# Kernel tuning notes

Hardware: AMD Instinct MI355X
Metric: run time of the kernel (lower is better)

The kernel has to match this reference:

```python
import jax, jax.numpy as jnp
import numpy as np
from jax import lax

BLANK = 27
NEG = -1e30  # safe -inf substitute (avoids NaN grads through logaddexp)


def _joint_log_probs(enc, dec, We, Wd, bf, Wp, bp):
    # Concat-then-Linear == sum of per-branch matmuls: [e;d] @ Wf = e@We + d@Wd.
    f = jnp.einsum('bte,eh->bth', enc, We)          # [B,T,H]
    g = jnp.einsum('bud,dh->buh', dec, Wd)          # [B,U1,H]
    h = jnp.tanh(f[:, :, None, :] + g[:, None, :, :] + bf)  # [B,T,U1,H]
    logits = jnp.einsum('btuh,hv->btuv', h, Wp) + bp         # [B,T,U1,V]
    return jax.nn.log_softmax(logits, axis=-1)


def _rnnt_loss_one(lp, tgt, t_len, u_len):
    # lp: [T,U1,V] log-probs, tgt: [U] int labels, t_len/u_len: scalars.
    T, U1, V = lp.shape
    blank_lp = lp[:, :, BLANK]                                   # [T,U1]
    lab_lp = jnp.take_along_axis(lp[:, :U1 - 1, :],
                                 tgt[None, :, None], axis=2)[..., 0]  # [T,U]

    # alpha[0,:] : only label emissions along u at t=0.
    alpha0 = jnp.concatenate([jnp.zeros((1,), lp.dtype),
                              jnp.cumsum(lab_lp[0])])            # [U1]

    def step(prev_alpha, inp):
        b_prev, lab_t = inp                       # [U1], [U]
        from_below = prev_alpha + b_prev          # blank move from t-1
        first = from_below[0]

        def inner(carry, x):
            fb, lab = x
            new = jnp.logaddexp(fb, carry + lab)  # blank-from-below vs label-from-left
            return new, new

        _, rest = lax.scan(inner, first, (from_below[1:], lab_t))
        alpha_t = jnp.concatenate([first[None], rest])
        return alpha_t, alpha_t

    _, alphas = lax.scan(step, alpha0, (blank_lp[:-1], lab_lp[1:]))
    alpha = jnp.concatenate([alpha0[None], alphas], axis=0)      # [T,U1]

    # Terminal: emit final blank at (t_len-1, u_len).
    return -(alpha[t_len - 1, u_len] + blank_lp[t_len - 1, u_len])


def setup_inputs() -> dict:
    key = jax.random.key(0)
    ks = jax.random.split(key, 10)
    B, T, U, E, D, H, V = 8, 400, 60, 256, 256, 512, 28
    enc_state = jax.random.normal(ks[0], (B, T, E), jnp.float32)
    dec_state = jax.random.normal(ks[1], (B, U + 1, D), jnp.float32)
    targets = jax.random.randint(ks[2], (B, U), 0, BLANK, jnp.int32)
    inputs_length = jax.random.randint(ks[3], (B,), 200, T + 1, jnp.int32)
    targets_length = jax.random.randint(ks[4], (B,), 30, U + 1, jnp.int32)
    s1 = 1.0 / np.sqrt(E + D)
    s2 = 1.0 / np.sqrt(H)
    We = jax.random.normal(ks[5], (E, H), jnp.float32) * s1
    Wd = jax.random.normal(ks[6], (D, H), jnp.float32) * s1
    bf = jax.random.normal(ks[7], (H,), jnp.float32) * s1
    Wp = jax.random.normal(ks[8], (H, V), jnp.float32) * s2
    bp = jax.random.normal(ks[9], (V,), jnp.float32) * s2
    return {"enc_state": enc_state, "dec_state": dec_state,
            "We": We, "Wd": Wd, "bf": bf, "Wp": Wp, "bp": bp,
            "targets": targets, "inputs_length": inputs_length,
            "targets_length": targets_length}


def reference(enc_state, dec_state, We, Wd, bf, Wp, bp,
              targets, inputs_length, targets_length):
    lp = _joint_log_probs(enc_state, dec_state, We, Wd, bf, Wp, bp)
    loss = jax.vmap(_rnnt_loss_one)(lp, targets, inputs_length, targets_length)
    return loss  # [B], reduction='none'
```

## Files before the change

### kernel.cpp

```cpp
#include <hip/hip_runtime.h>
#include <hip/hip_bf16.h>
#include <math.h>

#define NEGF (-1e30f)
#define LOG2E 1.4426950408889634f
#define LN2F 0.6931471805599453f
#define TSCALE 2.885390081777927f

typedef __attribute__((ext_vector_type(8))) short bf16x8;
typedef __attribute__((ext_vector_type(4))) float f32x4;

#define DROWS_PAD 480
#define DPITCH 64
#define PF 16

__device__ __forceinline__ unsigned short f2bf(float x) {
    __hip_bfloat16 h = __float2bfloat16(x);
    return *reinterpret_cast<unsigned short*>(&h);
}

__device__ __forceinline__ float wave_shr1(float x) {
    int i = __builtin_bit_cast(int, x);
    int r = __builtin_amdgcn_update_dpp(0, i, 0x138, 0xf, 0xf, true);
    return __builtin_bit_cast(float, r);
}

__device__ __forceinline__ float4 rcp4_nr(float4 d) {
    float4 y;
    y.x = __builtin_bit_cast(float, 0x7EF311C3 - __builtin_bit_cast(int, d.x));
    y.y = __builtin_bit_cast(float, 0x7EF311C3 - __builtin_bit_cast(int, d.y));
    y.z = __builtin_bit_cast(float, 0x7EF311C3 - __builtin_bit_cast(int, d.z));
    y.w = __builtin_bit_cast(float, 0x7EF311C3 - __builtin_bit_cast(int, d.w));
    float4 t;
    t.x = fmaf(-d.x, y.x, 2.f); t.y = fmaf(-d.y, y.y, 2.f);
    t.z = fmaf(-d.z, y.z, 2.f); t.w = fmaf(-d.w, y.w, 2.f);
    y.x *= t.x; y.y *= t.y; y.z *= t.z; y.w *= t.w;
    return y;
}

__global__ __launch_bounds__(256) void k_pack(const float* __restrict__ We,
                                              const float* __restrict__ Wd,
                                              const float* __restrict__ Wp,
                                              const float* __restrict__ bp,
                                              unsigned short* __restrict__ WeFrag,
                                              unsigned short* __restrict__ WdFrag,
                                              unsigned short* __restrict__ BfragP,
                                              float* __restrict__ csbp) {
    int gid = blockIdx.x * 256 + threadIdx.x;
    if (gid < 32768) {
        const float* W = (gid < 16384) ? We : Wd;
        unsigned short* F = (gid < 16384) ? WeFrag : WdFrag;
        int s = gid & 16383;
        int lane = s & 63;
        int c = (s >> 6) & 7;
        int nt = s >> 9;
        int n = nt * 16 + (lane & 15);
        int kbase = c * 32 + ((lane >> 4) & 3) * 8;
        unsigned short* dst = F + (size_t)s * 8;
#pragma unroll
        for (int j = 0; j < 8; ++j) dst[j] = f2bf(W[(size_t)(kbase + j) * 512 + n]);
    } else if (gid < 34816) {
        int s = gid - 32768;
        int lane = s & 63;
        int half = (s >> 6) & 1;
        int c = s >> 7;
        int n = half * 16 + (lane & 15);
        int kbase = c * 32 + (lane >> 4) * 8;
        unsigned short* dst = BfragP + (size_t)s * 8;
#pragma unroll
        for (int j = 0; j < 8; ++j) {
            float v = (n < 28) ? (-2.f * Wp[(kbase + j) * 28 + n]) : 0.f;
            dst[j] = f2bf(v);
        }
    } else if (gid < 34848) {
        int v = gid - 34816;
        float s = 0.f;
        if (v < 28) {
            for (int k = 0; k < 512; ++k) s += Wp[k * 28 + v];
            s += bp[v];
        }
        csbp[v] = s;
    }
}

__global__ __launch_bounds__(256) void k_gemm(const float* __restrict__ enc,
                                              const float* __restrict__ dec,
                                              const float* __restrict__ bfv,
                                              const unsigned short* __restrict__ WeFrag,
                                              const unsigned short* __restrict__ WdFrag,
                                              float* __restrict__ f,
                                              float* __restrict__ g) {
    const int wid = blockIdx.x * 4 + threadIdx.y;
    const int lane = threadIdx.x;
    const int m16 = lane & 15;
    const int quad = lane >> 4;

    const float* A; const unsigned short* WF; float* Out; int M, rt, ct; bool isg;
    if (wid < 1600) { A = enc; WF = WeFrag; Out = f; M = 3200; rt = wid >> 3; ct = wid & 7; isg = false; }
    else { int w2 = wid - 1600; A = dec; WF = WdFrag; Out = g; M = 488; rt = w2 >> 3; ct = w2 & 7; isg = true; }

    const int row = rt * 16 + m16;
    const float* arow = A + (size_t)min(row, M - 1) * 256 + quad * 8;

    f32x4 acc[4];
#pragma unroll
    for (int i = 0; i < 4; ++i) acc[i] = (f32x4){0.f, 0.f, 0.f, 0.f};

#pragma unroll
    for (int c = 0; c < 8; ++c) {
        float4 a0 = *(const float4*)(arow + c * 32);
        float4 a1 = *(const float4*)(arow + c * 32 + 4);
        union { unsigned short s[8]; bf16x8 v; } Af;
        Af.s[0] = f2bf(a0.x); Af.s[1] = f2bf(a0.y);
        Af.s[2] = f2bf(a0.z); Af.s[3] = f2bf(a0.w);
        Af.s[4] = f2bf(a1.x); Af.s[5] = f2bf(a1.y);
        Af.s[6] = f2bf(a1.z); Af.s[7] = f2bf(a1.w);
#pragma unroll
        for (int i = 0; i < 4; ++i) {
            int nt = ct * 4 + i;
            bf16x8 Bv = *(const bf16x8*)(WF + (size_t)((nt * 8 + c) * 64 + lane) * 8);
            acc[i] = __builtin_amdgcn_mfma_f32_16x16x32_bf16(Af.v, Bv, acc[i], 0, 0, 0);
        }
    }

#pragma unroll
    for (int i = 0; i < 4; ++i) {
        int n = ct * 64 + i * 16 + m16;
        float bv = isg ? bfv[n] : 0.f;
#pragma unroll
        for (int r = 0; r < 4; ++r) {
            int ro = rt * 16 + quad * 4 + r;
            if (ro < M) Out[(size_t)ro * 512 + n] = (acc[i][r] + bv) * TSCALE;
        }
    }
}

__global__ __launch_bounds__(256, 4) void k_cells(const float* __restrict__ f,
                                                  const float* __restrict__ g,
                                                  const unsigned short* __restrict__ Bfrag,
                                                  const float* __restrict__ csbp,
                                                  const int* __restrict__ targets,
                                                  const int* __restrict__ ilen,
                                                  const int* __restrict__ ulenp,
                                                  float2* __restrict__ pairD) {
    const int b = blockIdx.z;
    const int tlen = ilen[b];
    const int t0 = blockIdx.x * 16;
    if (t0 >= tlen) return;
    if ((int)blockIdx.y * 4 > ulenp[b]) return;
    const int wave = threadIdx.y;
    const int lane = threadIdx.x;
    const int u_raw = blockIdx.y * 4 + wave;
    const int u = min(u_raw, 60);
    const int tid = wave * 64 + lane;

    __shared__ float fs[16 * 516];

    {
        const float4* src = (const float4*)(f + (size_t)(b * 400 + t0) * 512);
#pragma unroll
        for (int i = 0; i < 8; ++i) {
            int idx = tid + i * 256;
            int row = idx >> 7;
            int c4 = idx & 127;
            float4 v = src[idx];
            *(float4*)&fs[row * 516 + c4 * 4] = v;
        }
    }
    __syncthreads();

    const int quad = lane >> 4;
    const int m16 = lane & 15;
    const float* gu = g + (size_t)(b * 61 + u) * 512 + quad * 8;
    const float* fsrow = fs + m16 * 516 + quad * 8;
    f32x4 acc0 = {0.f, 0.f, 0.f, 0.f};
    f32x4 acc1 = {0.f, 0.f, 0.f, 0.f};
    const float4 one4 = make_float4(1.f, 1.f, 1.f, 1.f);

    float4 FA[2], FB[2], GA[2], GB[2];
    bf16x8 BR0[2], BR1[2];
    FA[0] = *(const float4*)(fsrow);
    FB[0] = *(const float4*)(fsrow + 4);
    GA[0] = *(const float4*)(gu);
    GB[0] = *(const float4*)(gu + 4);
    BR0[0] = *(const bf16x8*)(Bfrag + ((size_t)(0 * 64 + lane)) * 8);
    BR1[0] = *(const bf16x8*)(Bfrag + ((size_t)(1 * 64 + lane)) * 8);

#pragma unroll
    for (int c = 0; c < 16; ++c) {
        const int cu = c & 1;
        const int nx = cu ^ 1;
        if (c < 15) {
            FA[nx] = *(const float4*)(fsrow + (c + 1) * 32);
            FB[nx] = *(const float4*)(fsrow + (c + 1) * 32 + 4);
            GA[nx] = *(const float4*)(gu + (c + 1) * 32);
            GB[nx] = *(const float4*)(gu + (c + 1) * 32 + 4);
            BR0[nx] = *(const bf16x8*)(Bfrag + ((size_t)(((c + 1) * 2 + 0) * 64 + lane)) * 8);
            BR1[nx] = *(const bf16x8*)(Bfrag + ((size_t)(((c + 1) * 2 + 1) * 64 + lane)) * 8);
        }
        float4 s0 = FA[cu] + GA[cu];
        float4 s1 = FB[cu] + GB[cu];
        float4 e0, e1;
        e0.x = __builtin_amdgcn_exp2f(s0.x); e0.y = __builtin_amdgcn_exp2f(s0.y);
        e0.z = __builtin_amdgcn_exp2f(s0.z); e0.w = __builtin_amdgcn_exp2f(s0.w);
        e1.x = __builtin_amdgcn_exp2f(s1.x); e1.y = __builtin_amdgcn_exp2f(s1.y);
        e1.z = __builtin_amdgcn_exp2f(s1.z); e1.w = __builtin_amdgcn_exp2f(s1.w);
        float4 r0 = rcp4_nr(e0 + one4);
        float4 r1 = rcp4_nr(e1 + one4);
        union { unsigned short s[8]; bf16x8 v; } A;
        A.s[0] = f2bf(r0.x); A.s[1] = f2bf(r0.y);
        A.s[2] = f2bf(r0.z); A.s[3] = f2bf(r0.w);
        A.s[4] = f2bf(r1.x); A.s[5] = f2bf(r1.y);
        A.s[6] = f2bf(r1.z); A.s[7] = f2bf(r1.w);
        acc0 = __builtin_amdgcn_mfma_f32_16x16x32_bf16(A.v, BR0[cu], acc0, 0, 0, 0);
        acc1 = __builtin_amdgcn_mfma_f32_16x16x32_bf16(A.v, BR1[cu], acc1, 0, 0, 0);
    }

    float cs0 = csbp[m16];
    int n1 = 16 + m16;
    bool n1v = (n1 < 28);
    float cs1 = csbp[n1 & 31];
    int tv = targets[b * 60 + min(u, 59)];

    float res_blank[4], res_lab[4];
#pragma unroll
    for (int r = 0; r < 4; ++r) {
        float l0 = acc0[r] + cs0;
        float l1 = n1v ? (acc1[r] + cs1) : NEGF;
        float mx = fmaxf(l0, l1);
        mx = fmaxf(mx, __shfl_xor(mx, 1, 64));
        mx = fmaxf(mx, __shfl_xor(mx, 2, 64));
        mx = fmaxf(mx, __shfl_xor(mx, 4, 64));
        mx = fmaxf(mx, __shfl_xor(mx, 8, 64));
        float s = __builtin_amdgcn_exp2f((l0 - mx) * LOG2E) +
                  __builtin_amdgcn_exp2f((l1 - mx) * LOG2E);
        s += __shfl_xor(s, 1, 64);
        s += __shfl_xor(s, 2, 64);
        s += __shfl_xor(s, 4, 64);
        s += __shfl_xor(s, 8, 64);
        float lse = mx + __logf(s);
        int base = lane & 48;
        float labsrc = (tv < 16) ? l0 : l1;
        float labv = __shfl(labsrc, base | (tv & 15), 64);
        float blankv = __shfl(l1, base | 11, 64);
        res_blank[r] = (blankv - lse) * LOG2E;
        res_lab[r] = (labv - lse) * LOG2E;
    }

    if (m16 == 0 && u_raw <= 60) {
        float2* Pd = pairD + (size_t)b * (DROWS_PAD * DPITCH);
#pragma unroll
        for (int r = 0; r < 4; ++r) {
            int t = t0 + quad * 4 + r;
            if (t < tlen) {
                int d = t + u;
                float2 pr;
                pr.x = res_blank[r];
                pr.y = (u <= 59) ? res_lab[r] : NEGF;
                Pd[d * DPITCH + u] = pr;
            }
        }
    }
}

__global__ __launch_bounds__(64) void k_alpha(const float2* __restrict__ pairD,
                                              const int* __restrict__ ilen,
                                              const int* __restrict__ ulenp,
                                              float* __restrict__ out) {
    const int b = blockIdx.x;
    const int u = threadIdx.x;
    const float2* Pd = pairD + (size_t)b * (DROWS_PAD * DPITCH);
    const int tl = ilen[b];
    const int ul = ulenp[b];
    const int dstar = tl - 1 + ul;
    const int dmax = ((dstar + PF - 1) / PF) * PF;
    const bool uok = (u <= 60);
    const bool lok = (u >= 1 && u <= 60);

    float cur = (u == 0) ? 0.f : NEGF;
    float saved = NEGF, savedBlank = NEGF;

    float2 pf[PF];
#pragma unroll
    for (int i = 0; i < PF; ++i) pf[i] = Pd[i * DPITCH + u];

    for (int d0 = 1; d0 <= dmax; d0 += PF) {
#pragma unroll
        for (int i = 0; i < PF; ++i) {
            const int d = d0 + i;
            float2 v = pf[i];
            pf[i] = Pd[(d + PF - 1) * DPITCH + u];
            int t = d - u;
            float bv = (t >= 1 && t <= 399 && uok) ? v.x : NEGF;
            float lvn = wave_shr1(v.y);
            float lv = (lok && t >= 0 && t <= 399) ? lvn : NEGF;
            float up = wave_shr1(cur);
            float a = cur + bv;
            float c2 = up + lv;
            float mx = fmaxf(a, c2), mn = fminf(a, c2);
            float nv = mx + __log2f(1.f + __builtin_amdgcn_exp2f(mn - mx));
            bool valid = (t >= 0 && t <= 399 && uok);
            cur = valid ? nv : cur;
            saved = (d == dstar) ? cur : saved;
            savedBlank = (d == dstar) ? v.x : savedBlank;
        }
    }
    if (u == ul) out[b] = -(saved + savedBlank) * LN2F;
}

extern "C" void kernel_launch(void* const* d_in, const int* in_sizes, int n_in,
                              void* d_out, int out_size, void* d_ws, size_t ws_size,
                              hipStream_t stream) {
    const float* enc = (const float*)d_in[0];
    const float* dec = (const float*)d_in[1];
    const float* We  = (const float*)d_in[2];
    const float* Wd  = (const float*)d_in[3];
    const float* bf  = (const float*)d_in[4];
    const float* Wp  = (const float*)d_in[5];
    const float* bp  = (const float*)d_in[6];
    const int* targets = (const int*)d_in[7];
    const int* ilen    = (const int*)d_in[8];
    const int* ulen    = (const int*)d_in[9];
    float* out = (float*)d_out;
    float* ws = (float*)d_ws;

    float* f     = ws;
    float* g     = ws + 1638400;
    unsigned short* BfragP = (unsigned short*)(ws + 1888256);
    unsigned short* WeFrag = (unsigned short*)(ws + 1896448);
    unsigned short* WdFrag = (unsigned short*)(ws + 1961984);
    float* csbp  = ws + 2027520;
    float2* pairD = (float2*)(ws + 2027552);

    k_pack<<<137, 256, 0, stream>>>(We, Wd, Wp, bp, WeFrag, WdFrag, BfragP, csbp);

    k_gemm<<<462, dim3(64, 4, 1), 0, stream>>>(enc, dec, bf, WeFrag, WdFrag, f, g);

    dim3 gridC(25, 16, 8);
    dim3 blockC(64, 4, 1);
    k_cells<<<gridC, blockC, 0, stream>>>(f, g, BfragP, csbp, targets, ilen, ulen, pairD);

    k_alpha<<<8, 64, 0, stream>>>(pairD, ilen, ulen, out);
}
```

Before: 148.8 us.

## Reuse staged f tile across 16 u per block; two-step alpha diagonal recurrence

k_cells now has each block loop over four groups of 4 u-values, so the 16x512 f tile staged in shared memory is reused for 16 u instead of 4. The grid's y-dimension shrinks from 16 to 4 to match. This cuts redundant global-to-LDS loads of f but leaves fewer blocks in flight and adds a serial loop inside each block. k_alpha now advances two anti-diagonals per step with a three-term logsumexp, roughly halving the serial dependency chain at the cost of more arithmetic per step, and it special-cases the terminal diagonal.

```diff
diff --git a/kernel.cpp b/kernel.cpp
--- a/kernel.cpp
+++ b/kernel.cpp
@@ -145,13 +145,12 @@
                                                   float2* __restrict__ pairD) {
     const int b = blockIdx.z;
     const int tlen = ilen[b];
+    const int ulen = ulenp[b];
     const int t0 = blockIdx.x * 16;
     if (t0 >= tlen) return;
-    if ((int)blockIdx.y * 4 > ulenp[b]) return;
+    if ((int)blockIdx.y * 16 > ulen) return;
     const int wave = threadIdx.y;
     const int lane = threadIdx.x;
-    const int u_raw = blockIdx.y * 4 + wave;
-    const int u = min(u_raw, 60);
     const int tid = wave * 64 + lane;
 
     __shared__ float fs[16 * 516];
@@ -171,93 +170,101 @@
 
     const int quad = lane >> 4;
     const int m16 = lane & 15;
-    const float* gu = g + (size_t)(b * 61 + u) * 512 + quad * 8;
     const float* fsrow = fs + m16 * 516 + quad * 8;
-    f32x4 acc0 = {0.f, 0.f, 0.f, 0.f};
-    f32x4 acc1 = {0.f, 0.f, 0.f, 0.f};
     const float4 one4 = make_float4(1.f, 1.f, 1.f, 1.f);
-
-    float4 FA[2], FB[2], GA[2], GB[2];
-    bf16x8 BR0[2], BR1[2];
-    FA[0] = *(const float4*)(fsrow);
-    FB[0] = *(const float4*)(fsrow + 4);
-    GA[0] = *(const float4*)(gu);
-    GB[0] = *(const float4*)(gu + 4);
-    BR0[0] = *(const bf16x8*)(Bfrag + ((size_t)(0 * 64 + lane)) * 8);
-    BR1[0] = *(const bf16x8*)(Bfrag + ((size_t)(1 * 64 + lane)) * 8);
-
-#pragma unroll
-    for (int c = 0; c < 16; ++c) {
-        const int cu = c & 1;
-        const int nx = cu ^ 1;
-        if (c < 15) {
-            FA[nx] = *(const float4*)(fsrow + (c + 1) * 32);
-            FB[nx] = *(const float4*)(fsrow + (c + 1) * 32 + 4);
-            GA[nx] = *(const float4*)(gu + (c + 1) * 32);
-            GB[nx] = *(const float4*)(gu + (c + 1) * 32 + 4);
-            BR0[nx] = *(const bf16x8*)(Bfrag + ((size_t)(((c + 1) * 2 + 0) * 64 + lane)) * 8);
-            BR1[nx] = *(const bf16x8*)(Bfrag + ((size_t)(((c + 1) * 2 + 1) * 64 + lane)) * 8);
-        }
-        float4 s0 = FA[cu] + GA[cu];
-        float4 s1 = FB[cu] + GB[cu];
-        float4 e0, e1;
-        e0.x = __builtin_amdgcn_exp2f(s0.x); e0.y = __builtin_amdgcn_exp2f(s0.y);
-        e0.z = __builtin_amdgcn_exp2f(s0.z); e0.w = __builtin_amdgcn_exp2f(s0.w);
-        e1.x = __builtin_amdgcn_exp2f(s1.x); e1.y = __builtin_amdgcn_exp2f(s1.y);
-        e1.z = __builtin_amdgcn_exp2f(s1.z); e1.w = __builtin_amdgcn_exp2f(s1.w);
-        float4 r0 = rcp4_nr(e0 + one4);
-        float4 r1 = rcp4_nr(e1 + one4);
-        union { unsigned short s[8]; bf16x8 v; } A;
-        A.s[0] = f2bf(r0.x); A.s[1] = f2bf(r0.y);
-        A.s[2] = f2bf(r0.z); A.s[3] = f2bf(r0.w);
-        A.s[4] = f2bf(r1.x); A.s[5] = f2bf(r1.y);
-        A.s[6] = f2bf(r1.z); A.s[7] = f2bf(r1.w);
-        acc0 = __builtin_amdgcn_mfma_f32_16x16x32_bf16(A.v, BR0[cu], acc0, 0, 0, 0);
-        acc1 = __builtin_amdgcn_mfma_f32_16x16x32_bf16(A.v, BR1[cu], acc1, 0, 0, 0);
-    }
-
-    float cs0 = csbp[m16];
-    int n1 = 16 + m16;
-    bool n1v = (n1 < 28);
-    float cs1 = csbp[n1 & 31];
-    int tv = targets[b * 60 + min(u, 59)];
-
-    float res_blank[4], res_lab[4];
-#pragma unroll
-    for (int r = 0; r < 4; ++r) {
-        float l0 = acc0[r] + cs0;
-        float l1 = n1v ? (acc1[r] + cs1) : NEGF;
-        float mx = fmaxf(l0, l1);
-        mx = fmaxf(mx, __shfl_xor(mx, 1, 64));
-        mx = fmaxf(mx, __shfl_xor(mx, 2, 64));
-        mx = fmaxf(mx, __shfl_xor(mx, 4, 64));
-        mx = fmaxf(mx, __shfl_xor(mx, 8, 64));
-        float s = __builtin_amdgcn_exp2f((l0 - mx) * LOG2E) +
-                  __builtin_amdgcn_exp2f((l1 - mx) * LOG2E);
-        s += __shfl_xor(s, 1, 64);
-        s += __shfl_xor(s, 2, 64);
-        s += __shfl_xor(s, 4, 64);
-        s += __shfl_xor(s, 8, 64);
-        float lse = mx + __logf(s);
-        int base = lane & 48;
-        float labsrc = (tv < 16) ? l0 : l1;
-        float labv = __shfl(labsrc, base | (tv & 15), 64);
-        float blankv = __shfl(l1, base | 11, 64);
-        res_blank[r] = (blankv - lse) * LOG2E;
-        res_lab[r] = (labv - lse) * LOG2E;
-    }
-
-    if (m16 == 0 && u_raw <= 60) {
-        float2* Pd = pairD + (size_t)b * (DROWS_PAD * DPITCH);
+    const float cs0 = csbp[m16];
+    const int n1 = 16 + m16;
+    const bool n1v = (n1 < 28);
+    const float cs1 = csbp[n1 & 31];
+    float2* Pd = pairD + (size_t)b * (DROWS_PAD * DPITCH);
+
+    for (int ub = 0; ub < 4; ++ub) {
+        const int ubase = blockIdx.y * 16 + ub * 4;
+        if (ubase > ulen) break;
+        const int u_raw = ubase + wave;
+        const int u = min(u_raw, 60);
+        const float* gu = g + (size_t)(b * 61 + u) * 512 + quad * 8;
+
+        f32x4 acc0 = {0.f, 0.f, 0.f, 0.f};
+        f32x4 acc1 = {0.f, 0.f, 0.f, 0.f};
+
+        float4 FA[2], FB[2], GA[2], GB[2];
+        bf16x8 BR0[2], BR1[2];
+        FA[0] = *(const float4*)(fsrow);
+        FB[0] = *(const float4*)(fsrow + 4);
+        GA[0] = *(const float4*)(gu);
+        GB[0] = *(const float4*)(gu + 4);
+        BR0[0] = *(const bf16x8*)(Bfrag + ((size_t)(0 * 64 + lane)) * 8);
+        BR1[0] = *(const bf16x8*)(Bfrag + ((size_t)(1 * 64 + lane)) * 8);
+
+#pragma unroll
+        for (int c = 0; c < 16; ++c) {
+            const int cu = c & 1;
+            const int nx = cu ^ 1;
+            if (c < 15) {
+                FA[nx] = *(const float4*)(fsrow + (c + 1) * 32);
+                FB[nx] = *(const float4*)(fsrow + (c + 1) * 32 + 4);
+                GA[nx] = *(const float4*)(gu + (c + 1) * 32);
+                GB[nx] = *(const float4*)(gu + (c + 1) * 32 + 4);
+                BR0[nx] = *(const bf16x8*)(Bfrag + ((size_t)(((c + 1) * 2 + 0) * 64 + lane)) * 8);
+                BR1[nx] = *(const bf16x8*)(Bfrag + ((size_t)(((c + 1) * 2 + 1) * 64 + lane)) * 8);
+            }
+            float4 s0 = FA[cu] + GA[cu];
+            float4 s1 = FB[cu] + GB[cu];
+            float4 e0, e1;
+            e0.x = __builtin_amdgcn_exp2f(s0.x); e0.y = __builtin_amdgcn_exp2f(s0.y);
+            e0.z = __builtin_amdgcn_exp2f(s0.z); e0.w = __builtin_amdgcn_exp2f(s0.w);
+            e1.x = __builtin_amdgcn_exp2f(s1.x); e1.y = __builtin_amdgcn_exp2f(s1.y);
+            e1.z = __builtin_amdgcn_exp2f(s1.z); e1.w = __builtin_amdgcn_exp2f(s1.w);
+            float4 r0 = rcp4_nr(e0 + one4);
+            float4 r1 = rcp4_nr(e1 + one4);
+            union { unsigned short s[8]; bf16x8 v; } A;
+            A.s[0] = f2bf(r0.x); A.s[1] = f2bf(r0.y);
+            A.s[2] = f2bf(r0.z); A.s[3] = f2bf(r0.w);
+            A.s[4] = f2bf(r1.x); A.s[5] = f2bf(r1.y);
+            A.s[6] = f2bf(r1.z); A.s[7] = f2bf(r1.w);
+            acc0 = __builtin_amdgcn_mfma_f32_16x16x32_bf16(A.v, BR0[cu], acc0, 0, 0, 0);
+            acc1 = __builtin_amdgcn_mfma_f32_16x16x32_bf16(A.v, BR1[cu], acc1, 0, 0, 0);
+        }
+
+        int tv = targets[b * 60 + min(u, 59)];
+
+        float res_blank[4], res_lab[4];
 #pragma unroll
         for (int r = 0; r < 4; ++r) {
-            int t = t0 + quad * 4 + r;
-            if (t < tlen) {
-                int d = t + u;
-                float2 pr;
-                pr.x = res_blank[r];
-                pr.y = (u <= 59) ? res_lab[r] : NEGF;
-                Pd[d * DPITCH + u] = pr;
+            float l0 = acc0[r] + cs0;
+            float l1 = n1v ? (acc1[r] + cs1) : NEGF;
+            float mx = fmaxf(l0, l1);
+            mx = fmaxf(mx, __shfl_xor(mx, 1, 64));
+            mx = fmaxf(mx, __shfl_xor(mx, 2, 64));
+            mx = fmaxf(mx, __shfl_xor(mx, 4, 64));
+            mx = fmaxf(mx, __shfl_xor(mx, 8, 64));
+            float s = __builtin_amdgcn_exp2f((l0 - mx) * LOG2E) +
+                      __builtin_amdgcn_exp2f((l1 - mx) * LOG2E);
+            s += __shfl_xor(s, 1, 64);
+            s += __shfl_xor(s, 2, 64);
+            s += __shfl_xor(s, 4, 64);
+            s += __shfl_xor(s, 8, 64);
+            float lse = mx + __logf(s);
+            int base = lane & 48;
+            float labsrc = (tv < 16) ? l0 : l1;
+            float labv = __shfl(labsrc, base | (tv & 15), 64);
+            float blankv = __shfl(l1, base | 11, 64);
+            res_blank[r] = (blankv - lse) * LOG2E;
+            res_lab[r] = (labv - lse) * LOG2E;
+        }
+
+        if (m16 == 0 && u_raw <= 60) {
+#pragma unroll
+            for (int r = 0; r < 4; ++r) {
+                int t = t0 + quad * 4 + r;
+                if (t < tlen) {
+                    int d = t + u;
+                    float2 pr;
+                    pr.x = res_blank[r];
+                    pr.y = (u <= 59) ? res_lab[r] : NEGF;
+                    Pd[d * DPITCH + u] = pr;
+                }
             }
         }
     }
@@ -278,7 +285,7 @@
     const bool lok = (u >= 1 && u <= 60);
 
     float cur = (u == 0) ? 0.f : NEGF;
-    float saved = NEGF, savedBlank = NEGF;
+    float saved = NEGF;
 
     float2 pf[PF];
 #pragma unroll
@@ -286,26 +293,46 @@
 
     for (int d0 = 1; d0 <= dmax; d0 += PF) {
 #pragma unroll
-        for (int i = 0; i < PF; ++i) {
-            const int d = d0 + i;
-            float2 v = pf[i];
-            pf[i] = Pd[(d + PF - 1) * DPITCH + u];
-            int t = d - u;
-            float bv = (t >= 1 && t <= 399 && uok) ? v.x : NEGF;
-            float lvn = wave_shr1(v.y);
-            float lv = (lok && t >= 0 && t <= 399) ? lvn : NEGF;
-            float up = wave_shr1(cur);
-            float a = cur + bv;
-            float c2 = up + lv;
-            float mx = fmaxf(a, c2), mn = fminf(a, c2);
-            float nv = mx + __log2f(1.f + __builtin_amdgcn_exp2f(mn - mx));
-            bool valid = (t >= 0 && t <= 399 && uok);
-            cur = valid ? nv : cur;
-            saved = (d == dstar) ? cur : saved;
-            savedBlank = (d == dstar) ? v.x : savedBlank;
-        }
-    }
-    if (u == ul) out[b] = -(saved + savedBlank) * LN2F;
+        for (int i = 0; i < PF / 2; ++i) {
+            const int d = d0 + 2 * i;
+            float2 v1 = pf[2 * i];
+            float2 v2 = pf[2 * i + 1];
+            pf[2 * i]     = Pd[(d + PF - 1) * DPITCH + u];
+            pf[2 * i + 1] = Pd[(d + PF)     * DPITCH + u];
+            const int t1 = d - u;
+            const int t2 = t1 + 1;
+            float bv1 = (t1 >= 1 && t1 <= 399 && uok) ? v1.x : NEGF;
+            float lv1 = (lok && t1 >= 0 && t1 <= 399) ? wave_shr1(v1.y) : NEGF;
+            float bv2 = (t2 >= 1 && t2 <= 399 && uok) ? v2.x : NEGF;
+            float lv2 = (lok && t2 >= 0 && t2 <= 399) ? wave_shr1(v2.y) : NEGF;
+            float A = bv1 + bv2;
+            float bv1s = wave_shr1(bv1);
+            float lv1s = wave_shr1(lv1);
+            float p1 = lv1 + bv2, p2 = bv1s + lv2;
+            float pmx = fmaxf(p1, p2), pmn = fminf(p1, p2);
+            float Bc = pmx + __log2f(1.f + __builtin_amdgcn_exp2f(pmn - pmx));
+            float C = lv1s + lv2;
+            float sh1 = wave_shr1(cur);
+            float sh2 = wave_shr1(sh1);
+            float a1 = cur + A;
+            float a2 = sh1 + Bc;
+            float a3 = sh2 + C;
+            float mx = fmaxf(fmaxf(a1, a2), a3);
+            float s = __builtin_amdgcn_exp2f(a1 - mx)
+                    + __builtin_amdgcn_exp2f(a2 - mx)
+                    + __builtin_amdgcn_exp2f(a3 - mx);
+            float nv = mx + __log2f(s);
+            if ((unsigned)(dstar - d) <= 1u) {
+                float xa = cur + bv1;
+                float xb = sh1 + lv1;
+                float xmx = fmaxf(xa, xb), xmn = fminf(xa, xb);
+                float x = xmx + __log2f(1.f + __builtin_amdgcn_exp2f(xmn - xmx));
+                saved = (d == dstar) ? x : nv;
+            }
+            cur = nv;
+        }
+    }
+    if (u == ul) out[b] = -(saved + Pd[dstar * DPITCH + u].x) * LN2F;
 }
 
 extern "C" void kernel_launch(void* const* d_in, const int* in_sizes, int n_in,
@@ -336,7 +363,7 @@
 
     k_gemm<<<462, dim3(64, 4, 1), 0, stream>>>(enc, dec, bf, WeFrag, WdFrag, f, g);
 
-    dim3 gridC(25, 16, 8);
+    dim3 gridC(25, 4, 8);
     dim3 blockC(64, 4, 1);
     k_cells<<<gridC, blockC, 0, stream>>>(f, g, BfragP, csbp, targets, ilen, ulen, pairD);
 
```

Result: slower. 165.6 us (+11.3%).

## Reuse f tile across 16 u per block and stage alpha diagonals through LDS

Applied to the files above, without the earlier changes.

k_cells now loops over four u-groups per block, so the shared-memory f tile loaded once is reused for 16 label positions instead of 4, and the grid shrinks along y. k_alpha becomes a 256-thread block in which three producer waves double-buffer 48-diagonal chunks of pairD into LDS while wave 0 runs the serial alpha recurrence reading from LDS. The aim is to cut redundant f loads and to hide global-memory latency in the serial recurrence. The costs are fewer blocks for k_cells, serialized u-groups within each block, and a block barrier per chunk in k_alpha.

```diff
diff --git a/kernel.cpp b/kernel.cpp
--- a/kernel.cpp
+++ b/kernel.cpp
@@ -12,7 +12,7 @@
 
 #define DROWS_PAD 480
 #define DPITCH 64
-#define PF 16
+#define CH 48
 
 __device__ __forceinline__ unsigned short f2bf(float x) {
     __hip_bfloat16 h = __float2bfloat16(x);
@@ -145,13 +145,12 @@
                                                   float2* __restrict__ pairD) {
     const int b = blockIdx.z;
     const int tlen = ilen[b];
+    const int ulen = ulenp[b];
     const int t0 = blockIdx.x * 16;
     if (t0 >= tlen) return;
-    if ((int)blockIdx.y * 4 > ulenp[b]) return;
+    if ((int)blockIdx.y * 16 > ulen) return;
     const int wave = threadIdx.y;
     const int lane = threadIdx.x;
-    const int u_raw = blockIdx.y * 4 + wave;
-    const int u = min(u_raw, 60);
     const int tid = wave * 64 + lane;
 
     __shared__ float fs[16 * 516];
@@ -171,141 +170,169 @@
 
     const int quad = lane >> 4;
     const int m16 = lane & 15;
-    const float* gu = g + (size_t)(b * 61 + u) * 512 + quad * 8;
     const float* fsrow = fs + m16 * 516 + quad * 8;
-    f32x4 acc0 = {0.f, 0.f, 0.f, 0.f};
-    f32x4 acc1 = {0.f, 0.f, 0.f, 0.f};
     const float4 one4 = make_float4(1.f, 1.f, 1.f, 1.f);
-
-    float4 FA[2], FB[2], GA[2], GB[2];
-    bf16x8 BR0[2], BR1[2];
-    FA[0] = *(const float4*)(fsrow);
-    FB[0] = *(const float4*)(fsrow + 4);
-    GA[0] = *(const float4*)(gu);
-    GB[0] = *(const float4*)(gu + 4);
-    BR0[0] = *(const bf16x8*)(Bfrag + ((size_t)(0 * 64 + lane)) * 8);
-    BR1[0] = *(const bf16x8*)(Bfrag + ((size_t)(1 * 64 + lane)) * 8);
-
-#pragma unroll
-    for (int c = 0; c < 16; ++c) {
-        const int cu = c & 1;
-        const int nx = cu ^ 1;
-        if (c < 15) {
-            FA[nx] = *(const float4*)(fsrow + (c + 1) * 32);
-            FB[nx] = *(const float4*)(fsrow + (c + 1) * 32 + 4);
-            GA[nx] = *(const float4*)(gu + (c + 1) * 32);
-            GB[nx] = *(const float4*)(gu + (c + 1) * 32 + 4);
-            BR0[nx] = *(const bf16x8*)(Bfrag + ((size_t)(((c + 1) * 2 + 0) * 64 + lane)) * 8);
-            BR1[nx] = *(const bf16x8*)(Bfrag + ((size_t)(((c + 1) * 2 + 1) * 64 + lane)) * 8);
-        }
-        float4 s0 = FA[cu] + GA[cu];
-        float4 s1 = FB[cu] + GB[cu];
-        float4 e0, e1;
-        e0.x = __builtin_amdgcn_exp2f(s0.x); e0.y = __builtin_amdgcn_exp2f(s0.y);
-        e0.z = __builtin_amdgcn_exp2f(s0.z); e0.w = __builtin_amdgcn_exp2f(s0.w);
-        e1.x = __builtin_amdgcn_exp2f(s1.x); e1.y = __builtin_amdgcn_exp2f(s1.y);
-        e1.z = __builtin_amdgcn_exp2f(s1.z); e1.w = __builtin_amdgcn_exp2f(s1.w);
-        float4 r0 = rcp4_nr(e0 + one4);
-        float4 r1 = rcp4_nr(e1 + one4);
-        union { unsigned short s[8]; bf16x8 v; } A;
-        A.s[0] = f2bf(r0.x); A.s[1] = f2bf(r0.y);
-        A.s[2] = f2bf(r0.z); A.s[3] = f2bf(r0.w);
-        A.s[4] = f2bf(r1.x); A.s[5] = f2bf(r1.y);
-        A.s[6] = f2bf(r1.z); A.s[7] = f2bf(r1.w);
-        acc0 = __builtin_amdgcn_mfma_f32_16x16x32_bf16(A.v, BR0[cu], acc0, 0, 0, 0);
-        acc1 = __builtin_amdgcn_mfma_f32_16x16x32_bf16(A.v, BR1[cu], acc1, 0, 0, 0);
-    }
-
-    float cs0 = csbp[m16];
-    int n1 = 16 + m16;
-    bool n1v = (n1 < 28);
-    float cs1 = csbp[n1 & 31];
-    int tv = targets[b * 60 + min(u, 59)];
-
-    float res_blank[4], res_lab[4];
-#pragma unroll
-    for (int r = 0; r < 4; ++r) {
-        float l0 = acc0[r] + cs0;
-        float l1 = n1v ? (acc1[r] + cs1) : NEGF;
-        float mx = fmaxf(l0, l1);
-        mx = fmaxf(mx, __shfl_xor(mx, 1, 64));
-        mx = fmaxf(mx, __shfl_xor(mx, 2, 64));
-        mx = fmaxf(mx, __shfl_xor(mx, 4, 64));
-        mx = fmaxf(mx, __shfl_xor(mx, 8, 64));
-        float s = __builtin_amdgcn_exp2f((l0 - mx) * LOG2E) +
-                  __builtin_amdgcn_exp2f((l1 - mx) * LOG2E);
-        s += __shfl_xor(s, 1, 64);
-        s += __shfl_xor(s, 2, 64);
-        s += __shfl_xor(s, 4, 64);
-        s += __shfl_xor(s, 8, 64);
-        float lse = mx + __logf(s);
-        int base = lane & 48;
-        float labsrc = (tv < 16) ? l0 : l1;
-        float labv = __shfl(labsrc, base | (tv & 15), 64);
-        float blankv = __shfl(l1, base | 11, 64);
-        res_blank[r] = (blankv - lse) * LOG2E;
-        res_lab[r] = (labv - lse) * LOG2E;
-    }
-
-    if (m16 == 0 && u_raw <= 60) {
-        float2* Pd = pairD + (size_t)b * (DROWS_PAD * DPITCH);
+    const float cs0 = csbp[m16];
+    const int n1 = 16 + m16;
+    const bool n1v = (n1 < 28);
+    const float cs1 = csbp[n1 & 31];
+    float2* Pd = pairD + (size_t)b * (DROWS_PAD * DPITCH);
+
+    for (int ub = 0; ub < 4; ++ub) {
+        const int ubase = blockIdx.y * 16 + ub * 4;
+        if (ubase > ulen) break;
+        const int u_raw = ubase + wave;
+        const int u = min(u_raw, 60);
+        const float* gu = g + (size_t)(b * 61 + u) * 512 + quad * 8;
+
+        f32x4 acc0 = {0.f, 0.f, 0.f, 0.f};
+        f32x4 acc1 = {0.f, 0.f, 0.f, 0.f};
+
+        float4 FA[2], FB[2], GA[2], GB[2];
+        bf16x8 BR0[2], BR1[2];
+        FA[0] = *(const float4*)(fsrow);
+        FB[0] = *(const float4*)(fsrow + 4);
+        GA[0] = *(const float4*)(gu);
+        GB[0] = *(const float4*)(gu + 4);
+        BR0[0] = *(const bf16x8*)(Bfrag + ((size_t)(0 * 64 + lane)) * 8);
+        BR1[0] = *(const bf16x8*)(Bfrag + ((size_t)(1 * 64 + lane)) * 8);
+
+#pragma unroll
+        for (int c = 0; c < 16; ++c) {
+            const int cu = c & 1;
+            const int nx = cu ^ 1;
+            if (c < 15) {
+                FA[nx] = *(const float4*)(fsrow + (c + 1) * 32);
+                FB[nx] = *(const float4*)(fsrow + (c + 1) * 32 + 4);
+                GA[nx] = *(const float4*)(gu + (c + 1) * 32);
+                GB[nx] = *(const float4*)(gu + (c + 1) * 32 + 4);
+                BR0[nx] = *(const bf16x8*)(Bfrag + ((size_t)(((c + 1) * 2 + 0) * 64 + lane)) * 8);
+                BR1[nx] = *(const bf16x8*)(Bfrag + ((size_t)(((c + 1) * 2 + 1) * 64 + lane)) * 8);
+            }
+            float4 s0 = FA[cu] + GA[cu];
+            float4 s1 = FB[cu] + GB[cu];
+            float4 e0, e1;
+            e0.x = __builtin_amdgcn_exp2f(s0.x); e0.y = __builtin_amdgcn_exp2f(s0.y);
+            e0.z = __builtin_amdgcn_exp2f(s0.z); e0.w = __builtin_amdgcn_exp2f(s0.w);
+            e1.x = __builtin_amdgcn_exp2f(s1.x); e1.y = __builtin_amdgcn_exp2f(s1.y);
+            e1.z = __builtin_amdgcn_exp2f(s1.z); e1.w = __builtin_amdgcn_exp2f(s1.w);
+            float4 r0 = rcp4_nr(e0 + one4);
+            float4 r1 = rcp4_nr(e1 + one4);
+            union { unsigned short s[8]; bf16x8 v; } A;
+            A.s[0] = f2bf(r0.x); A.s[1] = f2bf(r0.y);
+            A.s[2] = f2bf(r0.z); A.s[3] = f2bf(r0.w);
+            A.s[4] = f2bf(r1.x); A.s[5] = f2bf(r1.y);
+            A.s[6] = f2bf(r1.z); A.s[7] = f2bf(r1.w);
+            acc0 = __builtin_amdgcn_mfma_f32_16x16x32_bf16(A.v, BR0[cu], acc0, 0, 0, 0);
+            acc1 = __builtin_amdgcn_mfma_f32_16x16x32_bf16(A.v, BR1[cu], acc1, 0, 0, 0);
+        }
+
+        int tv = targets[b * 60 + min(u, 59)];
+
+        float res_blank[4], res_lab[4];
 #pragma unroll
         for (int r = 0; r < 4; ++r) {
-            int t = t0 + quad * 4 + r;
-            if (t < tlen) {
-                int d = t + u;
-                float2 pr;
-                pr.x = res_blank[r];
-                pr.y = (u <= 59) ? res_lab[r] : NEGF;
-                Pd[d * DPITCH + u] = pr;
+            float l0 = acc0[r] + cs0;
+            float l1 = n1v ? (acc1[r] + cs1) : NEGF;
+            float mx = fmaxf(l0, l1);
+            mx = fmaxf(mx, __shfl_xor(mx, 1, 64));
+            mx = fmaxf(mx, __shfl_xor(mx, 2, 64));
+            mx = fmaxf(mx, __shfl_xor(mx, 4, 64));
+            mx = fmaxf(mx, __shfl_xor(mx, 8, 64));
+            float s = __builtin_amdgcn_exp2f((l0 - mx) * LOG2E) +
+                      __builtin_amdgcn_exp2f((l1 - mx) * LOG2E);
+            s += __shfl_xor(s, 1, 64);
+            s += __shfl_xor(s, 2, 64);
+            s += __shfl_xor(s, 4, 64);
+            s += __shfl_xor(s, 8, 64);
+            float lse = mx + __logf(s);
+            int base = lane & 48;
+            float labsrc = (tv < 16) ? l0 : l1;
+            float labv = __shfl(labsrc, base | (tv & 15), 64);
+            float blankv = __shfl(l1, base | 11, 64);
+            res_blank[r] = (blankv - lse) * LOG2E;
+            res_lab[r] = (labv - lse) * LOG2E;
+        }
+
+        if (m16 == 0 && u_raw <= 60) {
+#pragma unroll
+            for (int r = 0; r < 4; ++r) {
+                int t = t0 + quad * 4 + r;
+                if (t < tlen) {
+                    int d = t + u;
+                    float2 pr;
+                    pr.x = res_blank[r];
+                    pr.y = (u <= 59) ? res_lab[r] : NEGF;
+                    Pd[d * DPITCH + u] = pr;
+                }
             }
         }
     }
 }
 
-__global__ __launch_bounds__(64) void k_alpha(const float2* __restrict__ pairD,
-                                              const int* __restrict__ ilen,
-                                              const int* __restrict__ ulenp,
-                                              float* __restrict__ out) {
+__global__ __launch_bounds__(256) void k_alpha(const float2* __restrict__ pairD,
+                                               const int* __restrict__ ilen,
+                                               const int* __restrict__ ulenp,
+                                               float* __restrict__ out) {
     const int b = blockIdx.x;
     const int u = threadIdx.x;
+    const int w = threadIdx.y;
     const float2* Pd = pairD + (size_t)b * (DROWS_PAD * DPITCH);
     const int tl = ilen[b];
     const int ul = ulenp[b];
     const int dstar = tl - 1 + ul;
-    const int dmax = ((dstar + PF - 1) / PF) * PF;
+    const int NCH = (dstar + CH - 1) / CH;
     const bool uok = (u <= 60);
     const bool lok = (u >= 1 && u <= 60);
 
+    __shared__ char lbuf[2 * CH * 512];
+
+    {
+        const int tid = w * 64 + u;
+        const float4* gs = (const float4*)Pd;
+        float4* ld = (float4*)lbuf;
+#pragma unroll
+        for (int j = 0; j < 6; ++j) ld[tid + j * 256] = gs[tid + j * 256];
+    }
+    __syncthreads();
+
     float cur = (u == 0) ? 0.f : NEGF;
     float saved = NEGF, savedBlank = NEGF;
 
-    float2 pf[PF];
-#pragma unroll
-    for (int i = 0; i < PF; ++i) pf[i] = Pd[i * DPITCH + u];
-
-    for (int d0 = 1; d0 <= dmax; d0 += PF) {
-#pragma unroll
-        for (int i = 0; i < PF; ++i) {
-            const int d = d0 + i;
-            float2 v = pf[i];
-            pf[i] = Pd[(d + PF - 1) * DPITCH + u];
-            int t = d - u;
-            float bv = (t >= 1 && t <= 399 && uok) ? v.x : NEGF;
-            float lvn = wave_shr1(v.y);
-            float lv = (lok && t >= 0 && t <= 399) ? lvn : NEGF;
-            float up = wave_shr1(cur);
-            float a = cur + bv;
-            float c2 = up + lv;
-            float mx = fmaxf(a, c2), mn = fminf(a, c2);
-            float nv = mx + __log2f(1.f + __builtin_amdgcn_exp2f(mn - mx));
-            bool valid = (t >= 0 && t <= 399 && uok);
-            cur = valid ? nv : cur;
-            saved = (d == dstar) ? cur : saved;
-            savedBlank = (d == dstar) ? v.x : savedBlank;
-        }
-    }
-    if (u == ul) out[b] = -(saved + savedBlank) * LN2F;
+    for (int k = 0; k < NCH; ++k) {
+        if (w > 0 && (k + 1) < NCH) {
+            const int pt = (w - 1) * 64 + u;
+            const float4* gs = (const float4*)(Pd + (size_t)(k + 1) * CH * DPITCH);
+            float4* ld = (float4*)(lbuf + ((k + 1) & 1) * (CH * 512));
+#pragma unroll
+            for (int j = 0; j < 8; ++j)
+                ld[pt + j * 192] = gs[pt + j * 192];
+        }
+        if (w == 0) {
+            const char* base = lbuf + (k & 1) * (CH * 512);
+            const int d0 = k * CH + 1;
+#pragma unroll 16
+            for (int r = 0; r < CH; ++r) {
+                const int d = d0 + r;
+                float2 v = *(const float2*)(base + r * 512 + u * 8);
+                int t = d - u;
+                float bv = (t >= 1 && t <= 399 && uok) ? v.x : NEGF;
+                float lvn = wave_shr1(v.y);
+                float lv = (lok && t >= 0 && t <= 399) ? lvn : NEGF;
+                float up = wave_shr1(cur);
+                float a = cur + bv;
+                float c2 = up + lv;
+                float mx = fmaxf(a, c2), mn = fminf(a, c2);
+                float nv = mx + __log2f(1.f + __builtin_amdgcn_exp2f(mn - mx));
+                bool valid = (t >= 0 && t <= 399 && uok);
+                cur = valid ? nv : cur;
+                saved = (d == dstar) ? cur : saved;
+                savedBlank = (d == dstar) ? v.x : savedBlank;
+            }
+        }
+        __syncthreads();
+    }
+    if (w == 0 && u == ul) out[b] = -(saved + savedBlank) * LN2F;
 }
 
 extern "C" void kernel_launch(void* const* d_in, const int* in_sizes, int n_in,
@@ -336,9 +363,9 @@
 
     k_gemm<<<462, dim3(64, 4, 1), 0, stream>>>(enc, dec, bf, WeFrag, WdFrag, f, g);
 
-    dim3 gridC(25, 16, 8);
+    dim3 gridC(25, 4, 8);
     dim3 blockC(64, 4, 1);
     k_cells<<<gridC, blockC, 0, stream>>>(f, g, BfragP, csbp, targets, ilen, ulen, pairD);
 
-    k_alpha<<<8, 64, 0, stream>>>(pairD, ilen, ulen, out);
-}
+    k_alpha<<<8, dim3(64, 4, 1), 0, stream>>>(pairD, ilen, ulen, out);
+}
```

After: 150.7 us. No clear change (+1.3%).
